# Kernel tuning notes

Measured on AMD Instinct MI355X. Metric: run time of the kernel, lower is better.

## Reference

```python
import jax, jax.numpy as jnp
import numpy as np
from jax import lax

KD, KH, KW = 9, 9, 9  # box-filter window (matches torch ones([1,1,9,9,9]))


def _box_sum(x):
    """Sum over a 9x9x9 window with SAME (zero) padding, via separable 1D convs.
    x: [B, 1, D, H, W]. Mathematically identical to conv3d with an all-ones
    9x9x9 kernel, but O(3k) instead of O(k^3) work per voxel.
    """
    dn = ('NCDHW', 'OIDHW', 'NCDHW')
    dt = x.dtype
    kd = jnp.ones((1, 1, KD, 1, 1), dt)
    kh = jnp.ones((1, 1, 1, KH, 1), dt)
    kw = jnp.ones((1, 1, 1, 1, KW), dt)
    pd, ph, pw = (KD - 1) // 2, (KH - 1) // 2, (KW - 1) // 2
    x = lax.conv_general_dilated(x, kd, (1, 1, 1), [(pd, pd), (0, 0), (0, 0)], dimension_numbers=dn)
    x = lax.conv_general_dilated(x, kh, (1, 1, 1), [(0, 0), (ph, ph), (0, 0)], dimension_numbers=dn)
    x = lax.conv_general_dilated(x, kw, (1, 1, 1), [(0, 0), (0, 0), (pw, pw)], dimension_numbers=dn)
    return x


def setup_inputs() -> dict:
    key = jax.random.key(0)
    k1, k2 = jax.random.split(key)
    shape = (2, 1, 160, 192, 160)  # [B, C=1, D, H, W]
    return {
        'input': jax.random.normal(k1, shape, dtype=jnp.float32),
        'target': jax.random.normal(k2, shape, dtype=jnp.float32),
    }


def reference(input, target):
    ksize = jnp.asarray(KD * KH * KW, input.dtype)
    I_sum = _box_sum(input)
    T_sum = _box_sum(target)
    II_sum = _box_sum(input * input)
    TT_sum = _box_sum(target * target)
    IT_sum = _box_sum(input * target)

    Ihat = I_sum / ksize
    That = T_sum / ksize
    cross = IT_sum - Ihat * T_sum - That * I_sum + That * Ihat * ksize
    T_var = TT_sum - 2 * That * T_sum + That * That * ksize
    I_var = II_sum - 2 * Ihat * I_sum + Ihat * Ihat * ksize
    cc = cross * cross / (T_var * I_var + 1e-5)
    return -1.0 * jnp.mean(cc)
```

## Files before the change

### kernel.cpp

```cpp
#include <hip/hip_runtime.h>

#define DIM_W 160
#define DIM_H 192
#define DIM_D 160
#define DIM_B 2

constexpr int TW = 16;
constexpr int TH = 32;
constexpr int CH = 28;
constexpr int NCH = 6;
constexpr int RH = TH + 8;
constexpr int RWDS = 24;
constexpr float INV_K = 1.0f / 729.0f;
constexpr double NTOT = 9830400.0;

typedef unsigned int u32;
typedef __attribute__((address_space(1))) const u32 gu32;
typedef __attribute__((address_space(3))) u32 lu32;

__global__ void init_kernel(float* out, float* ws) {
    out[0] = 0.0f;
    ws[0] = 0.0f; ws[1] = 0.0f; ws[2] = 0.0f; ws[3] = 0.0f;
}

__device__ __forceinline__ int clampD(int s) {
    return s < 0 ? 0 : (s > DIM_D - 1 ? DIM_D - 1 : s);
}

__global__ __launch_bounds__(256)
void lncc3d_kernel(const float* __restrict__ I,
                   const float* __restrict__ T,
                   const float* __restrict__ zsrc,
                   float* __restrict__ out)
{
    __shared__ __align__(16) float sR[2][2][1024];
    __shared__ __align__(16) float4 wA[RH][16];
    __shared__ __align__(16) float  wB[16][42];
    __shared__ float red[4];

    const int tid  = threadIdx.x;
    const int lane = tid & 63;
    const int wid  = tid >> 6;
    const int wo   = tid & 15;
    const int hb   = (tid >> 4) << 1;

    const int bw = blockIdx.x, bh = blockIdx.y, bz = blockIdx.z;
    const int b  = bz / NCH;
    const int c  = bz - b * NCH;
    const int w0 = bw * TW, h0 = bh * TH, d0 = c * CH;
    const int dEnd = min(d0 + CH, DIM_D);

    const int plane = DIM_H * DIM_W;
    const int fld = wid >> 1;
    const int khi = wid & 1;
    const float* Fb = (fld ? T : I) + (size_t)b * DIM_D * plane;

    int boff[2], ldof[2];
#pragma unroll
    for (int i = 0; i < 2; ++i) {
        const int ck  = (khi << 1) | i;
        const int s16 = ck * 64 + lane;
        const int row = s16 / 6;
        const int q   = s16 - row * 6;
        const int gh  = h0 - 4 + row;
        const int gw  = w0 - 4 + (q << 2);
        ldof[i] = ck << 8;
        boff[i] = (row < RH && gh >= 0 && gh < DIM_H && gw >= 0 && gw <= DIM_W - 4)
                  ? (gh * DIM_W + gw) : -1;
    }

    auto issue = [&](int sc, int buf) {
        const float* Fs = Fb + (size_t)sc * plane;
#pragma unroll
        for (int i = 0; i < 2; ++i) {
            const float* gp = (boff[i] >= 0) ? (Fs + boff[i]) : zsrc;
            __builtin_amdgcn_global_load_lds((gu32*)gp, (lu32*)&sR[buf][fld][ldof[i]],
                                             16, 0, 0);
        }
    };

    float rgI[2][9], rgT[2][9], rgII[2][9], rgTT[2][9], rgIT[2][9];
    float rnI[2], rnT[2], rnII[2], rnTT[2], rnIT[2];
#pragma unroll
    for (int p = 0; p < 2; ++p) {
        rnI[p] = rnT[p] = rnII[p] = rnTT[p] = rnIT[p] = 0.0f;
#pragma unroll
        for (int q = 0; q < 9; ++q) {
            rgI[p][q] = rgT[p][q] = rgII[p][q] = rgTT[p][q] = rgIT[p][q] = 0.0f;
        }
    }
    float acc = 0.0f;

    const int sStart = d0 - 4;
    int cur = 0;

    issue(clampD(sStart), 0);
    issue(clampD(sStart + 1), 1);
    asm volatile("s_waitcnt vmcnt(2)" ::: "memory");
    __builtin_amdgcn_s_barrier();

    for (int t = 0; t < 4; ++t) {
        const int t9 = t * 9;
#pragma unroll
        for (int j = 0; j < 9; ++j) {
            const int s  = sStart + t9 + j;
            const bool vs = (s >= 0) && (s < DIM_D);

            if (vs && tid < 160) {
                const int r  = tid >> 2;
                const int g  = tid & 3;
                const int c0 = g << 2;
                const float* rIp = &sR[cur][0][r * RWDS];
                const float* rTp = &sR[cur][1][r * RWDS];
                const float4 ia  = *(const float4*)(rIp + c0);
                const float4 ib4 = *(const float4*)(rIp + c0 + 4);
                const float4 ic4 = *(const float4*)(rIp + c0 + 8);
                const float4 ta  = *(const float4*)(rTp + c0);
                const float4 tb4 = *(const float4*)(rTp + c0 + 4);
                const float4 tc4 = *(const float4*)(rTp + c0 + 8);
                const float iv[12] = {ia.x, ia.y, ia.z, ia.w, ib4.x, ib4.y, ib4.z, ib4.w,
                                      ic4.x, ic4.y, ic4.z, ic4.w};
                const float tv[12] = {ta.x, ta.y, ta.z, ta.w, tb4.x, tb4.y, tb4.z, tb4.w,
                                      tc4.x, tc4.y, tc4.z, tc4.w};
                float aI = 0.f, aT = 0.f, aII = 0.f, aTT = 0.f, aIT = 0.f;
#pragma unroll
                for (int k = 0; k < 9; ++k) {
                    aI += iv[k]; aT += tv[k];
                    aII = fmaf(iv[k], iv[k], aII);
                    aTT = fmaf(tv[k], tv[k], aTT);
                    aIT = fmaf(iv[k], tv[k], aIT);
                }
                wA[r][(c0 + r) & 15] = make_float4(aI, aT, aII, aTT);
                wB[c0][r] = aIT;
#pragma unroll
                for (int q = 1; q < 4; ++q) {
                    const float ni = iv[8 + q], oi = iv[q - 1];
                    const float nt = tv[8 + q], ot = tv[q - 1];
                    aI += ni - oi; aT += nt - ot;
                    aII = fmaf(ni, ni, fmaf(oi, -oi, aII));
                    aTT = fmaf(nt, nt, fmaf(ot, -ot, aTT));
                    aIT = fmaf(ni, nt, fmaf(oi, -ot, aIT));
                    wA[r][(c0 + q + r) & 15] = make_float4(aI, aT, aII, aTT);
                    wB[c0 + q][r] = aIT;
                }
            }
            asm volatile("s_waitcnt lgkmcnt(0)" ::: "memory");
            __builtin_amdgcn_s_barrier();

            issue(clampD(s + 2), cur);

            float s2I0, s2T0, s2II0, s2TT0, s2IT0, s2I1, s2T1, s2II1, s2TT1, s2IT1;
            if (vs) {
                const float4 A0 = wA[hb][(wo + hb) & 15];
                float sx = A0.x, sy = A0.y, szv = A0.z, swv = A0.w;
#pragma unroll
                for (int k = 1; k < 9; ++k) {
                    const float4 Ak = wA[hb + k][(wo + hb + k) & 15];
                    sx += Ak.x; sy += Ak.y; szv += Ak.z; swv += Ak.w;
                }
                const float4 A9 = wA[hb + 9][(wo + hb + 9) & 15];
                const float2 B0 = *(const float2*)&wB[wo][hb];
                const float2 B1 = *(const float2*)&wB[wo][hb + 2];
                const float2 B2 = *(const float2*)&wB[wo][hb + 4];
                const float2 B3 = *(const float2*)&wB[wo][hb + 6];
                const float2 B4 = *(const float2*)&wB[wo][hb + 8];
                const float sbv = B0.x + B0.y + B1.x + B1.y + B2.x + B2.y
                                + B3.x + B3.y + B4.x;
                s2I0 = sx; s2T0 = sy; s2II0 = szv; s2TT0 = swv; s2IT0 = sbv;
                s2I1  = sx  - A0.x + A9.x;
                s2T1  = sy  - A0.y + A9.y;
                s2II1 = szv - A0.z + A9.z;
                s2TT1 = swv - A0.w + A9.w;
                s2IT1 = sbv - B0.x + B4.y;
            } else {
                s2I0 = s2T0 = s2II0 = s2TT0 = s2IT0 = 0.f;
                s2I1 = s2T1 = s2II1 = s2TT1 = s2IT1 = 0.f;
            }

            rnI[0]  += s2I0  - rgI[0][j];  rgI[0][j]  = s2I0;
            rnT[0]  += s2T0  - rgT[0][j];  rgT[0][j]  = s2T0;
            rnII[0] += s2II0 - rgII[0][j]; rgII[0][j] = s2II0;
            rnTT[0] += s2TT0 - rgTT[0][j]; rgTT[0][j] = s2TT0;
            rnIT[0] += s2IT0 - rgIT[0][j]; rgIT[0][j] = s2IT0;
            rnI[1]  += s2I1  - rgI[1][j];  rgI[1][j]  = s2I1;
            rnT[1]  += s2T1  - rgT[1][j];  rgT[1][j]  = s2T1;
            rnII[1] += s2II1 - rgII[1][j]; rgII[1][j] = s2II1;
            rnTT[1] += s2TT1 - rgTT[1][j]; rgTT[1][j] = s2TT1;
            rnIT[1] += s2IT1 - rgIT[1][j]; rgIT[1][j] = s2IT1;

            if ((s >= d0 + 4) && ((s - 4) < dEnd)) {
                float cr, vv, tvv;
                cr  = rnIT[0] - rnI[0] * rnT[0] * INV_K;
                vv  = rnII[0] - rnI[0] * rnI[0] * INV_K;
                tvv = rnTT[0] - rnT[0] * rnT[0] * INV_K;
                acc += cr * cr * __builtin_amdgcn_rcpf(fmaf(tvv, vv, 1e-5f));
                cr  = rnIT[1] - rnI[1] * rnT[1] * INV_K;
                vv  = rnII[1] - rnI[1] * rnI[1] * INV_K;
                tvv = rnTT[1] - rnT[1] * rnT[1] * INV_K;
                acc += cr * cr * __builtin_amdgcn_rcpf(fmaf(tvv, vv, 1e-5f));
            }

            asm volatile("s_waitcnt lgkmcnt(0)" ::: "memory");
            asm volatile("s_waitcnt vmcnt(2)" ::: "memory");
            __builtin_amdgcn_s_barrier();
            cur ^= 1;
        }
    }

#pragma unroll
    for (int off = 32; off > 0; off >>= 1) acc += __shfl_down(acc, off, 64);
    if (lane == 0) red[wid] = acc;
    __syncthreads();
    if (tid == 0) {
        const float bs = red[0] + red[1] + red[2] + red[3];
        atomicAdd(out, bs * (float)(-1.0 / NTOT));
    }
}

extern "C" void kernel_launch(void* const* d_in, const int* in_sizes, int n_in,
                              void* d_out, int out_size, void* d_ws, size_t ws_size,
                              hipStream_t stream) {
    const float* I = (const float*)d_in[0];
    const float* T = (const float*)d_in[1];
    float* out = (float*)d_out;
    float* ws  = (float*)d_ws;

    init_kernel<<<dim3(1), dim3(1), 0, stream>>>(out, ws);

    dim3 grid(DIM_W / TW, DIM_H / TH, DIM_B * NCH);
    dim3 block(256);
    lncc3d_kernel<<<grid, block, 0, stream>>>(I, T, ws, out);
}
```

Measured before the change: 86.33 us.

## Use DPP prefix-scan for H-direction box sum and retile blocks

Result: slower. 91.99 us (+6.6%).

```diff
diff --git a/kernel.cpp b/kernel.cpp
--- a/kernel.cpp
+++ b/kernel.cpp
@@ -6,10 +6,10 @@
 #define DIM_B 2
 
 constexpr int TW = 16;
-constexpr int TH = 32;
-constexpr int CH = 28;
-constexpr int NCH = 6;
-constexpr int RH = TH + 8;
+constexpr int TH = 24;
+constexpr int CH = 19;
+constexpr int NCH = 9;
+constexpr int RH = 32;
 constexpr int RWDS = 24;
 constexpr float INV_K = 1.0f / 729.0f;
 constexpr double NTOT = 9830400.0;
@@ -26,6 +26,23 @@
 __device__ __forceinline__ int clampD(int s) {
     return s < 0 ? 0 : (s > DIM_D - 1 ? DIM_D - 1 : s);
 }
+
+#define DPPF(v, ctrl) __builtin_bit_cast(float, \
+    __builtin_amdgcn_update_dpp(0, __builtin_bit_cast(int, (float)(v)), \
+                                (ctrl), 0xF, 0xF, true))
+
+#define SCAN5(S1, S2, S4, S8, SL4) \
+    _Pragma("unroll") \
+    for (int f = 0; f < 5; ++f) { \
+        float L = r0v[f] + r1v[f]; \
+        L += DPPF(L, S1); L += DPPF(L, S2); \
+        L += DPPF(L, S4); L += DPPF(L, S8); \
+        const float Pp4 = DPPF(L, SL4); \
+        const float Pm1 = DPPF(L, S1); \
+        const float r9v = DPPF(r1v[f], SL4); \
+        w0v[f] = Pp4 - r9v - Pm1; \
+        w1v[f] = Pp4 - Pm1 - r0v[f]; \
+    }
 
 __global__ __launch_bounds__(256)
 void lncc3d_kernel(const float* __restrict__ I,
@@ -33,16 +50,16 @@
                    const float* __restrict__ zsrc,
                    float* __restrict__ out)
 {
-    __shared__ __align__(16) float sR[2][2][1024];
+    __shared__ __align__(16) float sR[2][2][768];
     __shared__ __align__(16) float4 wA[RH][16];
-    __shared__ __align__(16) float  wB[16][42];
+    __shared__ __align__(16) float  wB[16][34];
     __shared__ float red[4];
 
     const int tid  = threadIdx.x;
     const int lane = tid & 63;
     const int wid  = tid >> 6;
-    const int wo   = tid & 15;
-    const int hb   = (tid >> 4) << 1;
+    const int wo   = tid >> 4;
+    const int i    = tid & 15;
 
     const int bw = blockIdx.x, bh = blockIdx.y, bz = blockIdx.z;
     const int b  = bz / NCH;
@@ -51,42 +68,47 @@
     const int dEnd = min(d0 + CH, DIM_D);
 
     const int plane = DIM_H * DIM_W;
-    const int fld = wid >> 1;
-    const int khi = wid & 1;
-    const float* Fb = (fld ? T : I) + (size_t)b * DIM_D * plane;
-
-    int boff[2], ldof[2];
-#pragma unroll
-    for (int i = 0; i < 2; ++i) {
-        const int ck  = (khi << 1) | i;
-        const int s16 = ck * 64 + lane;
+    const float* Ib = I + (size_t)b * DIM_D * plane;
+    const float* Tb = T + (size_t)b * DIM_D * plane;
+
+    const int shp = __builtin_amdgcn_update_dpp(0, lane, 0x104, 0xF, 0xF, true);
+    const bool dirA = (__builtin_amdgcn_readfirstlane(shp) == 4);
+
+    const bool ldw = (wid >= 2);
+    const int  fldg = (wid == 3);
+    const float* Fbg = fldg ? Tb : Ib;
+    int goff[3];
+#pragma unroll
+    for (int kk = 0; kk < 3; ++kk) {
+        const int s16 = kk * 64 + lane;
         const int row = s16 / 6;
         const int q   = s16 - row * 6;
         const int gh  = h0 - 4 + row;
         const int gw  = w0 - 4 + (q << 2);
-        ldof[i] = ck << 8;
-        boff[i] = (row < RH && gh >= 0 && gh < DIM_H && gw >= 0 && gw <= DIM_W - 4)
-                  ? (gh * DIM_W + gw) : -1;
+        goff[kk] = (gh >= 0 && gh < DIM_H && gw >= 0 && gw <= DIM_W - 4)
+                   ? (gh * DIM_W + gw) : -1;
     }
 
     auto issue = [&](int sc, int buf) {
-        const float* Fs = Fb + (size_t)sc * plane;
-#pragma unroll
-        for (int i = 0; i < 2; ++i) {
-            const float* gp = (boff[i] >= 0) ? (Fs + boff[i]) : zsrc;
-            __builtin_amdgcn_global_load_lds((gu32*)gp, (lu32*)&sR[buf][fld][ldof[i]],
-                                             16, 0, 0);
+        if (ldw) {
+            const float* Fs = Fbg + (size_t)sc * plane;
+#pragma unroll
+            for (int kk = 0; kk < 3; ++kk) {
+                const float* gp = (goff[kk] >= 0) ? (Fs + goff[kk]) : zsrc;
+                __builtin_amdgcn_global_load_lds((gu32*)gp,
+                    (lu32*)&sR[buf][fldg][kk << 8], 16, 0, 0);
+            }
         }
     };
 
-    float rgI[2][9], rgT[2][9], rgII[2][9], rgTT[2][9], rgIT[2][9];
-    float rnI[2], rnT[2], rnII[2], rnTT[2], rnIT[2];
+    float rg[2][5][9], rn[2][5];
 #pragma unroll
     for (int p = 0; p < 2; ++p) {
-        rnI[p] = rnT[p] = rnII[p] = rnTT[p] = rnIT[p] = 0.0f;
-#pragma unroll
-        for (int q = 0; q < 9; ++q) {
-            rgI[p][q] = rgT[p][q] = rgII[p][q] = rgTT[p][q] = rgIT[p][q] = 0.0f;
+#pragma unroll
+        for (int f = 0; f < 5; ++f) {
+            rn[p][f] = 0.0f;
+#pragma unroll
+            for (int q = 0; q < 9; ++q) rg[p][f][q] = 0.0f;
         }
     }
     float acc = 0.0f;
@@ -96,20 +118,21 @@
 
     issue(clampD(sStart), 0);
     issue(clampD(sStart + 1), 1);
-    asm volatile("s_waitcnt vmcnt(2)" ::: "memory");
+    if (ldw) { asm volatile("s_waitcnt vmcnt(3)" ::: "memory"); }
     __builtin_amdgcn_s_barrier();
 
-    for (int t = 0; t < 4; ++t) {
+    for (int t = 0; t < 3; ++t) {
         const int t9 = t * 9;
 #pragma unroll
         for (int j = 0; j < 9; ++j) {
             const int s  = sStart + t9 + j;
             const bool vs = (s >= 0) && (s < DIM_D);
 
-            if (vs && tid < 160) {
+            if (vs && tid < 128) {
                 const int r  = tid >> 2;
                 const int g  = tid & 3;
                 const int c0 = g << 2;
+                const int rr = r + (r >> 1);
                 const float* rIp = &sR[cur][0][r * RWDS];
                 const float* rTp = &sR[cur][1][r * RWDS];
                 const float4 ia  = *(const float4*)(rIp + c0);
@@ -130,7 +153,7 @@
                     aTT = fmaf(tv[k], tv[k], aTT);
                     aIT = fmaf(iv[k], tv[k], aIT);
                 }
-                wA[r][(c0 + r) & 15] = make_float4(aI, aT, aII, aTT);
+                wA[r][(c0 + rr) & 15] = make_float4(aI, aT, aII, aTT);
                 wB[c0][r] = aIT;
 #pragma unroll
                 for (int q = 1; q < 4; ++q) {
@@ -140,7 +163,7 @@
                     aII = fmaf(ni, ni, fmaf(oi, -oi, aII));
                     aTT = fmaf(nt, nt, fmaf(ot, -ot, aTT));
                     aIT = fmaf(ni, nt, fmaf(oi, -ot, aIT));
-                    wA[r][(c0 + q + r) & 15] = make_float4(aI, aT, aII, aTT);
+                    wA[r][(c0 + q + rr) & 15] = make_float4(aI, aT, aII, aTT);
                     wB[c0 + q][r] = aIT;
                 }
             }
@@ -149,59 +172,42 @@
 
             issue(clampD(s + 2), cur);
 
-            float s2I0, s2T0, s2II0, s2TT0, s2IT0, s2I1, s2T1, s2II1, s2TT1, s2IT1;
+            float w0v[5], w1v[5];
             if (vs) {
-                const float4 A0 = wA[hb][(wo + hb) & 15];
-                float sx = A0.x, sy = A0.y, szv = A0.z, swv = A0.w;
-#pragma unroll
-                for (int k = 1; k < 9; ++k) {
-                    const float4 Ak = wA[hb + k][(wo + hb + k) & 15];
-                    sx += Ak.x; sy += Ak.y; szv += Ak.z; swv += Ak.w;
-                }
-                const float4 A9 = wA[hb + 9][(wo + hb + 9) & 15];
-                const float2 B0 = *(const float2*)&wB[wo][hb];
-                const float2 B1 = *(const float2*)&wB[wo][hb + 2];
-                const float2 B2 = *(const float2*)&wB[wo][hb + 4];
-                const float2 B3 = *(const float2*)&wB[wo][hb + 6];
-                const float2 B4 = *(const float2*)&wB[wo][hb + 8];
-                const float sbv = B0.x + B0.y + B1.x + B1.y + B2.x + B2.y
-                                + B3.x + B3.y + B4.x;
-                s2I0 = sx; s2T0 = sy; s2II0 = szv; s2TT0 = swv; s2IT0 = sbv;
-                s2I1  = sx  - A0.x + A9.x;
-                s2T1  = sy  - A0.y + A9.y;
-                s2II1 = szv - A0.z + A9.z;
-                s2TT1 = swv - A0.w + A9.w;
-                s2IT1 = sbv - B0.x + B4.y;
+                float r0v[5], r1v[5];
+                const float4 A0 = wA[2 * i][(wo + 3 * i) & 15];
+                const float4 A1 = wA[2 * i + 1][(wo + 3 * i + 1) & 15];
+                const float2 Bv = *(const float2*)&wB[wo][2 * i];
+                r0v[0] = A0.x; r0v[1] = A0.y; r0v[2] = A0.z; r0v[3] = A0.w; r0v[4] = Bv.x;
+                r1v[0] = A1.x; r1v[1] = A1.y; r1v[2] = A1.z; r1v[3] = A1.w; r1v[4] = Bv.y;
+                if (dirA) {
+                    SCAN5(0x111, 0x112, 0x114, 0x118, 0x104)
+                } else {
+                    SCAN5(0x101, 0x102, 0x104, 0x108, 0x114)
+                }
             } else {
-                s2I0 = s2T0 = s2II0 = s2TT0 = s2IT0 = 0.f;
-                s2I1 = s2T1 = s2II1 = s2TT1 = s2IT1 = 0.f;
-            }
-
-            rnI[0]  += s2I0  - rgI[0][j];  rgI[0][j]  = s2I0;
-            rnT[0]  += s2T0  - rgT[0][j];  rgT[0][j]  = s2T0;
-            rnII[0] += s2II0 - rgII[0][j]; rgII[0][j] = s2II0;
-            rnTT[0] += s2TT0 - rgTT[0][j]; rgTT[0][j] = s2TT0;
-            rnIT[0] += s2IT0 - rgIT[0][j]; rgIT[0][j] = s2IT0;
-            rnI[1]  += s2I1  - rgI[1][j];  rgI[1][j]  = s2I1;
-            rnT[1]  += s2T1  - rgT[1][j];  rgT[1][j]  = s2T1;
-            rnII[1] += s2II1 - rgII[1][j]; rgII[1][j] = s2II1;
-            rnTT[1] += s2TT1 - rgTT[1][j]; rgTT[1][j] = s2TT1;
-            rnIT[1] += s2IT1 - rgIT[1][j]; rgIT[1][j] = s2IT1;
-
-            if ((s >= d0 + 4) && ((s - 4) < dEnd)) {
-                float cr, vv, tvv;
-                cr  = rnIT[0] - rnI[0] * rnT[0] * INV_K;
-                vv  = rnII[0] - rnI[0] * rnI[0] * INV_K;
-                tvv = rnTT[0] - rnT[0] * rnT[0] * INV_K;
-                acc += cr * cr * __builtin_amdgcn_rcpf(fmaf(tvv, vv, 1e-5f));
-                cr  = rnIT[1] - rnI[1] * rnT[1] * INV_K;
-                vv  = rnII[1] - rnI[1] * rnI[1] * INV_K;
-                tvv = rnTT[1] - rnT[1] * rnT[1] * INV_K;
-                acc += cr * cr * __builtin_amdgcn_rcpf(fmaf(tvv, vv, 1e-5f));
+#pragma unroll
+                for (int f = 0; f < 5; ++f) { w0v[f] = 0.f; w1v[f] = 0.f; }
+            }
+
+#pragma unroll
+            for (int f = 0; f < 5; ++f) {
+                rn[0][f] += w0v[f] - rg[0][f][j];  rg[0][f][j] = w0v[f];
+                rn[1][f] += w1v[f] - rg[1][f][j];  rg[1][f][j] = w1v[f];
+            }
+
+            if ((s >= d0 + 4) && ((s - 4) < dEnd) && (i < 12)) {
+#pragma unroll
+                for (int p = 0; p < 2; ++p) {
+                    const float cr  = rn[p][4] - rn[p][0] * rn[p][1] * INV_K;
+                    const float vv  = rn[p][2] - rn[p][0] * rn[p][0] * INV_K;
+                    const float tvv = rn[p][3] - rn[p][1] * rn[p][1] * INV_K;
+                    acc += cr * cr * __builtin_amdgcn_rcpf(fmaf(tvv, vv, 1e-5f));
+                }
             }
 
             asm volatile("s_waitcnt lgkmcnt(0)" ::: "memory");
-            asm volatile("s_waitcnt vmcnt(2)" ::: "memory");
+            if (ldw) { asm volatile("s_waitcnt vmcnt(3)" ::: "memory"); }
             __builtin_amdgcn_s_barrier();
             cur ^= 1;
         }
```

## Process two depth slices per barrier step, pack H-stage partials as fp16

Applied to the files above, without the earlier changes.

Result: no change. 85.93 us (-0.5%).

```diff
diff --git a/kernel.cpp b/kernel.cpp
--- a/kernel.cpp
+++ b/kernel.cpp
@@ -7,9 +7,9 @@
 
 constexpr int TW = 16;
 constexpr int TH = 32;
-constexpr int CH = 28;
-constexpr int NCH = 6;
-constexpr int RH = TH + 8;
+constexpr int CH = 19;
+constexpr int NCH = 9;
+constexpr int RH = 40;
 constexpr int RWDS = 24;
 constexpr float INV_K = 1.0f / 729.0f;
 constexpr double NTOT = 9830400.0;
@@ -17,6 +17,7 @@
 typedef unsigned int u32;
 typedef __attribute__((address_space(1))) const u32 gu32;
 typedef __attribute__((address_space(3))) u32 lu32;
+typedef _Float16 h2 __attribute__((ext_vector_type(2)));
 
 __global__ void init_kernel(float* out, float* ws) {
     out[0] = 0.0f;
@@ -26,6 +27,12 @@
 __device__ __forceinline__ int clampD(int s) {
     return s < 0 ? 0 : (s > DIM_D - 1 ? DIM_D - 1 : s);
 }
+
+__device__ __forceinline__ u32 pkf16(float a, float b) {
+    return __builtin_bit_cast(u32, __builtin_amdgcn_cvt_pkrtz(a, b));
+}
+
+struct S2 { float I0, T0, II0, TT0, IT0, I1, T1, II1, TT1, IT1; };
 
 __global__ __launch_bounds__(256)
 void lncc3d_kernel(const float* __restrict__ I,
@@ -33,9 +40,9 @@
                    const float* __restrict__ zsrc,
                    float* __restrict__ out)
 {
-    __shared__ __align__(16) float sR[2][2][1024];
-    __shared__ __align__(16) float4 wA[RH][16];
-    __shared__ __align__(16) float  wB[16][42];
+    __shared__ __align__(16) float sR[2][2][2][1024];
+    __shared__ __align__(16) uint2 wA[2][RH][16];
+    __shared__ __align__(16) float wB[2][16][44];
     __shared__ float red[4];
 
     const int tid  = threadIdx.x;
@@ -51,32 +58,110 @@
     const int dEnd = min(d0 + CH, DIM_D);
 
     const int plane = DIM_H * DIM_W;
-    const int fld = wid >> 1;
-    const int khi = wid & 1;
-    const float* Fb = (fld ? T : I) + (size_t)b * DIM_D * plane;
-
-    int boff[2], ldof[2];
-#pragma unroll
-    for (int i = 0; i < 2; ++i) {
-        const int ck  = (khi << 1) | i;
-        const int s16 = ck * 64 + lane;
+    const float* Ib = I + (size_t)b * DIM_D * plane;
+    const float* Tb = T + (size_t)b * DIM_D * plane;
+
+    const int  sl0  = (tid >= 160) ? 1 : 0;
+    const int  rem0 = tid - (sl0 ? 160 : 0);
+    const int  r0   = rem0 >> 2, g0 = rem0 & 3;
+    const bool has2 = (tid < 64);
+    const int  r1   = 24 + (tid >> 2), g1 = tid & 3;
+
+    const int stg_sl  = wid >> 1;
+    const int stg_fld = wid & 1;
+    const float* Fbg = (stg_fld ? Tb : Ib);
+    int goff[4];
+#pragma unroll
+    for (int k = 0; k < 4; ++k) {
+        const int s16 = k * 64 + lane;
         const int row = s16 / 6;
         const int q   = s16 - row * 6;
         const int gh  = h0 - 4 + row;
         const int gw  = w0 - 4 + (q << 2);
-        ldof[i] = ck << 8;
-        boff[i] = (row < RH && gh >= 0 && gh < DIM_H && gw >= 0 && gw <= DIM_W - 4)
+        goff[k] = (row < RH && gh >= 0 && gh < DIM_H && gw >= 0 && gw <= DIM_W - 4)
                   ? (gh * DIM_W + gw) : -1;
     }
 
-    auto issue = [&](int sc, int buf) {
-        const float* Fs = Fb + (size_t)sc * plane;
-#pragma unroll
-        for (int i = 0; i < 2; ++i) {
-            const float* gp = (boff[i] >= 0) ? (Fs + boff[i]) : zsrc;
-            __builtin_amdgcn_global_load_lds((gu32*)gp, (lu32*)&sR[buf][fld][ldof[i]],
-                                             16, 0, 0);
-        }
+    auto issue = [&](int spair, int buf) {
+        const int sc = clampD(spair + stg_sl);
+        const float* Fs = Fbg + (size_t)sc * plane;
+#pragma unroll
+        for (int k = 0; k < 4; ++k) {
+            const float* gp = (goff[k] >= 0) ? (Fs + goff[k]) : zsrc;
+            __builtin_amdgcn_global_load_lds((gu32*)gp,
+                (lu32*)&sR[buf][stg_sl][stg_fld][k << 8], 16, 0, 0);
+        }
+    };
+
+    auto st1 = [&](int buf, int sl, int r, int g) {
+        const int c0 = g << 2;
+        const float* rIp = &sR[buf][sl][0][r * RWDS];
+        const float* rTp = &sR[buf][sl][1][r * RWDS];
+        const float4 ia  = *(const float4*)(rIp + c0);
+        const float4 ib4 = *(const float4*)(rIp + c0 + 4);
+        const float4 ic4 = *(const float4*)(rIp + c0 + 8);
+        const float4 ta  = *(const float4*)(rTp + c0);
+        const float4 tb4 = *(const float4*)(rTp + c0 + 4);
+        const float4 tc4 = *(const float4*)(rTp + c0 + 8);
+        const float iv[12] = {ia.x, ia.y, ia.z, ia.w, ib4.x, ib4.y, ib4.z, ib4.w,
+                              ic4.x, ic4.y, ic4.z, ic4.w};
+        const float tv[12] = {ta.x, ta.y, ta.z, ta.w, tb4.x, tb4.y, tb4.z, tb4.w,
+                              tc4.x, tc4.y, tc4.z, tc4.w};
+        float aI = 0.f, aT = 0.f, aII = 0.f, aTT = 0.f, aIT = 0.f;
+#pragma unroll
+        for (int k = 0; k < 9; ++k) {
+            aI += iv[k]; aT += tv[k];
+            aII = fmaf(iv[k], iv[k], aII);
+            aTT = fmaf(tv[k], tv[k], aTT);
+            aIT = fmaf(iv[k], tv[k], aIT);
+        }
+        wA[sl][r][(c0 + r) & 15] = make_uint2(pkf16(aI, aT), pkf16(aII, aTT));
+        wB[sl][c0][r] = aIT;
+#pragma unroll
+        for (int q = 1; q < 4; ++q) {
+            const float ni = iv[8 + q], oi = iv[q - 1];
+            const float nt = tv[8 + q], ot = tv[q - 1];
+            aI += ni - oi; aT += nt - ot;
+            aII = fmaf(ni, ni, fmaf(oi, -oi, aII));
+            aTT = fmaf(nt, nt, fmaf(ot, -ot, aTT));
+            aIT = fmaf(ni, nt, fmaf(oi, -ot, aIT));
+            wA[sl][r][(c0 + q + r) & 15] = make_uint2(pkf16(aI, aT), pkf16(aII, aTT));
+            wB[sl][c0 + q][r] = aIT;
+        }
+    };
+
+    auto st2 = [&](int sl, bool vsx) -> S2 {
+        S2 o;
+        if (vsx) {
+            const uint2 C0 = wA[sl][hb][(wo + hb) & 15];
+            const h2 A0a = __builtin_bit_cast(h2, C0.x);
+            const h2 A0b = __builtin_bit_cast(h2, C0.y);
+            h2 SA = A0a, SB = A0b;
+#pragma unroll
+            for (int k = 1; k < 9; ++k) {
+                const uint2 Ck = wA[sl][hb + k][(wo + hb + k) & 15];
+                SA += __builtin_bit_cast(h2, Ck.x);
+                SB += __builtin_bit_cast(h2, Ck.y);
+            }
+            const uint2 C9 = wA[sl][hb + 9][(wo + hb + 9) & 15];
+            const h2 P1A = SA - A0a + __builtin_bit_cast(h2, C9.x);
+            const h2 P1B = SB - A0b + __builtin_bit_cast(h2, C9.y);
+            o.I0 = (float)SA.x;  o.T0 = (float)SA.y;
+            o.II0 = (float)SB.x; o.TT0 = (float)SB.y;
+            o.I1 = (float)P1A.x; o.T1 = (float)P1A.y;
+            o.II1 = (float)P1B.x; o.TT1 = (float)P1B.y;
+            const float2 B0 = *(const float2*)&wB[sl][wo][hb];
+            const float2 B1 = *(const float2*)&wB[sl][wo][hb + 2];
+            const float2 B2 = *(const float2*)&wB[sl][wo][hb + 4];
+            const float2 B3 = *(const float2*)&wB[sl][wo][hb + 6];
+            const float2 B4 = *(const float2*)&wB[sl][wo][hb + 8];
+            o.IT0 = B0.x + B0.y + B1.x + B1.y + B2.x + B2.y + B3.x + B3.y + B4.x;
+            o.IT1 = o.IT0 - B0.x + B4.y;
+        } else {
+            o.I0 = o.T0 = o.II0 = o.TT0 = o.IT0 = 0.f;
+            o.I1 = o.T1 = o.II1 = o.TT1 = o.IT1 = 0.f;
+        }
+        return o;
     };
 
     float rgI[2][9], rgT[2][9], rgII[2][9], rgTT[2][9], rgIT[2][9];
@@ -90,122 +175,69 @@
         }
     }
     float acc = 0.0f;
-
     const int sStart = d0 - 4;
-    int cur = 0;
-
-    issue(clampD(sStart), 0);
-    issue(clampD(sStart + 1), 1);
-    asm volatile("s_waitcnt vmcnt(2)" ::: "memory");
+
+    issue(sStart, 0);
+    issue(sStart + 2, 1);
+    asm volatile("s_waitcnt vmcnt(4)" ::: "memory");
     __builtin_amdgcn_s_barrier();
 
-    for (int t = 0; t < 4; ++t) {
-        const int t9 = t * 9;
-#pragma unroll
-        for (int j = 0; j < 9; ++j) {
-            const int s  = sStart + t9 + j;
-            const bool vs = (s >= 0) && (s < DIM_D);
-
-            if (vs && tid < 160) {
-                const int r  = tid >> 2;
-                const int g  = tid & 3;
-                const int c0 = g << 2;
-                const float* rIp = &sR[cur][0][r * RWDS];
-                const float* rTp = &sR[cur][1][r * RWDS];
-                const float4 ia  = *(const float4*)(rIp + c0);
-                const float4 ib4 = *(const float4*)(rIp + c0 + 4);
-                const float4 ic4 = *(const float4*)(rIp + c0 + 8);
-                const float4 ta  = *(const float4*)(rTp + c0);
-                const float4 tb4 = *(const float4*)(rTp + c0 + 4);
-                const float4 tc4 = *(const float4*)(rTp + c0 + 8);
-                const float iv[12] = {ia.x, ia.y, ia.z, ia.w, ib4.x, ib4.y, ib4.z, ib4.w,
-                                      ic4.x, ic4.y, ic4.z, ic4.w};
-                const float tv[12] = {ta.x, ta.y, ta.z, ta.w, tb4.x, tb4.y, tb4.z, tb4.w,
-                                      tc4.x, tc4.y, tc4.z, tc4.w};
-                float aI = 0.f, aT = 0.f, aII = 0.f, aTT = 0.f, aIT = 0.f;
-#pragma unroll
-                for (int k = 0; k < 9; ++k) {
-                    aI += iv[k]; aT += tv[k];
-                    aII = fmaf(iv[k], iv[k], aII);
-                    aTT = fmaf(tv[k], tv[k], aTT);
-                    aIT = fmaf(iv[k], tv[k], aIT);
-                }
-                wA[r][(c0 + r) & 15] = make_float4(aI, aT, aII, aTT);
-                wB[c0][r] = aIT;
-#pragma unroll
-                for (int q = 1; q < 4; ++q) {
-                    const float ni = iv[8 + q], oi = iv[q - 1];
-                    const float nt = tv[8 + q], ot = tv[q - 1];
-                    aI += ni - oi; aT += nt - ot;
-                    aII = fmaf(ni, ni, fmaf(oi, -oi, aII));
-                    aTT = fmaf(nt, nt, fmaf(ot, -ot, aTT));
-                    aIT = fmaf(ni, nt, fmaf(oi, -ot, aIT));
-                    wA[r][(c0 + q + r) & 15] = make_float4(aI, aT, aII, aTT);
-                    wB[c0 + q][r] = aIT;
-                }
-            }
-            asm volatile("s_waitcnt lgkmcnt(0)" ::: "memory");
-            __builtin_amdgcn_s_barrier();
-
-            issue(clampD(s + 2), cur);
-
-            float s2I0, s2T0, s2II0, s2TT0, s2IT0, s2I1, s2T1, s2II1, s2TT1, s2IT1;
-            if (vs) {
-                const float4 A0 = wA[hb][(wo + hb) & 15];
-                float sx = A0.x, sy = A0.y, szv = A0.z, swv = A0.w;
-#pragma unroll
-                for (int k = 1; k < 9; ++k) {
-                    const float4 Ak = wA[hb + k][(wo + hb + k) & 15];
-                    sx += Ak.x; sy += Ak.y; szv += Ak.z; swv += Ak.w;
-                }
-                const float4 A9 = wA[hb + 9][(wo + hb + 9) & 15];
-                const float2 B0 = *(const float2*)&wB[wo][hb];
-                const float2 B1 = *(const float2*)&wB[wo][hb + 2];
-                const float2 B2 = *(const float2*)&wB[wo][hb + 4];
-                const float2 B3 = *(const float2*)&wB[wo][hb + 6];
-                const float2 B4 = *(const float2*)&wB[wo][hb + 8];
-                const float sbv = B0.x + B0.y + B1.x + B1.y + B2.x + B2.y
-                                + B3.x + B3.y + B4.x;
-                s2I0 = sx; s2T0 = sy; s2II0 = szv; s2TT0 = swv; s2IT0 = sbv;
-                s2I1  = sx  - A0.x + A9.x;
-                s2T1  = sy  - A0.y + A9.y;
-                s2II1 = szv - A0.z + A9.z;
-                s2TT1 = swv - A0.w + A9.w;
-                s2IT1 = sbv - B0.x + B4.y;
-            } else {
-                s2I0 = s2T0 = s2II0 = s2TT0 = s2IT0 = 0.f;
-                s2I1 = s2T1 = s2II1 = s2TT1 = s2IT1 = 0.f;
-            }
-
-            rnI[0]  += s2I0  - rgI[0][j];  rgI[0][j]  = s2I0;
-            rnT[0]  += s2T0  - rgT[0][j];  rgT[0][j]  = s2T0;
-            rnII[0] += s2II0 - rgII[0][j]; rgII[0][j] = s2II0;
-            rnTT[0] += s2TT0 - rgTT[0][j]; rgTT[0][j] = s2TT0;
-            rnIT[0] += s2IT0 - rgIT[0][j]; rgIT[0][j] = s2IT0;
-            rnI[1]  += s2I1  - rgI[1][j];  rgI[1][j]  = s2I1;
-            rnT[1]  += s2T1  - rgT[1][j];  rgT[1][j]  = s2T1;
-            rnII[1] += s2II1 - rgII[1][j]; rgII[1][j] = s2II1;
-            rnTT[1] += s2TT1 - rgTT[1][j]; rgTT[1][j] = s2TT1;
-            rnIT[1] += s2IT1 - rgIT[1][j]; rgIT[1][j] = s2IT1;
-
-            if ((s >= d0 + 4) && ((s - 4) < dEnd)) {
-                float cr, vv, tvv;
-                cr  = rnIT[0] - rnI[0] * rnT[0] * INV_K;
-                vv  = rnII[0] - rnI[0] * rnI[0] * INV_K;
-                tvv = rnTT[0] - rnT[0] * rnT[0] * INV_K;
-                acc += cr * cr * __builtin_amdgcn_rcpf(fmaf(tvv, vv, 1e-5f));
-                cr  = rnIT[1] - rnI[1] * rnT[1] * INV_K;
-                vv  = rnII[1] - rnI[1] * rnI[1] * INV_K;
-                tvv = rnTT[1] - rnT[1] * rnT[1] * INV_K;
-                acc += cr * cr * __builtin_amdgcn_rcpf(fmaf(tvv, vv, 1e-5f));
-            }
-
-            asm volatile("s_waitcnt lgkmcnt(0)" ::: "memory");
-            asm volatile("s_waitcnt vmcnt(2)" ::: "memory");
-            __builtin_amdgcn_s_barrier();
-            cur ^= 1;
-        }
-    }
+#define RING(S, J, EM) { \
+    rnI[0]  += S.I0  - rgI[0][J];  rgI[0][J]  = S.I0; \
+    rnT[0]  += S.T0  - rgT[0][J];  rgT[0][J]  = S.T0; \
+    rnII[0] += S.II0 - rgII[0][J]; rgII[0][J] = S.II0; \
+    rnTT[0] += S.TT0 - rgTT[0][J]; rgTT[0][J] = S.TT0; \
+    rnIT[0] += S.IT0 - rgIT[0][J]; rgIT[0][J] = S.IT0; \
+    rnI[1]  += S.I1  - rgI[1][J];  rgI[1][J]  = S.I1; \
+    rnT[1]  += S.T1  - rgT[1][J];  rgT[1][J]  = S.T1; \
+    rnII[1] += S.II1 - rgII[1][J]; rgII[1][J] = S.II1; \
+    rnTT[1] += S.TT1 - rgTT[1][J]; rgTT[1][J] = S.TT1; \
+    rnIT[1] += S.IT1 - rgIT[1][J]; rgIT[1][J] = S.IT1; \
+    if (EM) { \
+        float cr, vv, tvv; \
+        cr  = rnIT[0] - rnI[0] * rnT[0] * INV_K; \
+        vv  = rnII[0] - rnI[0] * rnI[0] * INV_K; \
+        tvv = rnTT[0] - rnT[0] * rnT[0] * INV_K; \
+        acc += cr * cr * __builtin_amdgcn_rcpf(fmaf(tvv, vv, 1e-5f)); \
+        cr  = rnIT[1] - rnI[1] * rnT[1] * INV_K; \
+        vv  = rnII[1] - rnI[1] * rnI[1] * INV_K; \
+        tvv = rnTT[1] - rnT[1] * rnT[1] * INV_K; \
+        acc += cr * cr * __builtin_amdgcn_rcpf(fmaf(tvv, vv, 1e-5f)); \
+    } }
+
+#define PAIR(PP, J0, J1, BUF) { \
+    const int sA = sStart + 2 * (PP); \
+    const int sB = sA + 1; \
+    const bool vsA = (sA >= 0) && (sA < DIM_D); \
+    const bool vsB = (sB >= 0) && (sB < DIM_D); \
+    const bool v0 = sl0 ? vsB : vsA; \
+    if (v0) st1((BUF), sl0, r0, g0); \
+    if (has2 && vsB) st1((BUF), 1, r1, g1); \
+    asm volatile("s_waitcnt lgkmcnt(0)" ::: "memory"); \
+    __builtin_amdgcn_s_barrier(); \
+    issue(sA + 4, (BUF)); \
+    { \
+        const S2 sa = st2(0, vsA); \
+        const S2 sb = st2(1, vsB); \
+        const bool emA = (sA >= d0 + 4) && ((sA - 4) < dEnd); \
+        const bool emB = (sB >= d0 + 4) && ((sB - 4) < dEnd); \
+        RING(sa, J0, emA); \
+        RING(sb, J1, emB); \
+    } \
+    asm volatile("s_waitcnt lgkmcnt(0)" ::: "memory"); \
+    asm volatile("s_waitcnt vmcnt(4)" ::: "memory"); \
+    __builtin_amdgcn_s_barrier(); \
+}
+
+    PAIR(0,  0, 1, 0)  PAIR(1,  2, 3, 1)  PAIR(2,  4, 5, 0)  PAIR(3,  6, 7, 1)
+    PAIR(4,  8, 0, 0)  PAIR(5,  1, 2, 1)  PAIR(6,  3, 4, 0)  PAIR(7,  5, 6, 1)
+    PAIR(8,  7, 8, 0)  PAIR(9,  0, 1, 1)  PAIR(10, 2, 3, 0)  PAIR(11, 4, 5, 1)
+    PAIR(12, 6, 7, 0)  PAIR(13, 8, 0, 1)
+
+#undef PAIR
+#undef RING
+
+    asm volatile("s_waitcnt vmcnt(0)" ::: "memory");
 
 #pragma unroll
     for (int off = 32; off > 0; off >>= 1) acc += __shfl_down(acc, off, 64);
```

## Store W-sums in packed fp16, shrink depth chunks, raise occupancy

Applied to the files above, without the earlier changes.

Measured after the change: 188.3 us. 118% more time.

```diff
diff --git a/kernel.cpp b/kernel.cpp
--- a/kernel.cpp
+++ b/kernel.cpp
@@ -7,9 +7,9 @@
 
 constexpr int TW = 16;
 constexpr int TH = 32;
-constexpr int CH = 28;
-constexpr int NCH = 6;
-constexpr int RH = TH + 8;
+constexpr int CH = 19;
+constexpr int NCH = 9;
+constexpr int RH = 40;
 constexpr int RWDS = 24;
 constexpr float INV_K = 1.0f / 729.0f;
 constexpr double NTOT = 9830400.0;
@@ -17,6 +17,7 @@
 typedef unsigned int u32;
 typedef __attribute__((address_space(1))) const u32 gu32;
 typedef __attribute__((address_space(3))) u32 lu32;
+typedef _Float16 h2 __attribute__((ext_vector_type(2)));
 
 __global__ void init_kernel(float* out, float* ws) {
     out[0] = 0.0f;
@@ -27,15 +28,19 @@
     return s < 0 ? 0 : (s > DIM_D - 1 ? DIM_D - 1 : s);
 }
 
-__global__ __launch_bounds__(256)
+__device__ __forceinline__ u32 pkf16(float a, float b) {
+    return __builtin_bit_cast(u32, __builtin_amdgcn_cvt_pkrtz(a, b));
+}
+
+__global__ __launch_bounds__(256, 6)
 void lncc3d_kernel(const float* __restrict__ I,
                    const float* __restrict__ T,
                    const float* __restrict__ zsrc,
                    float* __restrict__ out)
 {
     __shared__ __align__(16) float sR[2][2][1024];
-    __shared__ __align__(16) float4 wA[RH][16];
-    __shared__ __align__(16) float  wB[16][42];
+    __shared__ __align__(16) uint2 wA[RH][16];
+    __shared__ __align__(16) float wB[16][44];
     __shared__ float red[4];
 
     const int tid  = threadIdx.x;
@@ -53,7 +58,8 @@
     const int plane = DIM_H * DIM_W;
     const int fld = wid >> 1;
     const int khi = wid & 1;
-    const float* Fb = (fld ? T : I) + (size_t)b * DIM_D * plane;
+    const float* Fb = ((wid & 2) ? T : I) + (size_t)b * DIM_D * plane;
+    (void)fld;
 
     int boff[2], ldof[2];
 #pragma unroll
@@ -74,19 +80,21 @@
 #pragma unroll
         for (int i = 0; i < 2; ++i) {
             const float* gp = (boff[i] >= 0) ? (Fs + boff[i]) : zsrc;
-            __builtin_amdgcn_global_load_lds((gu32*)gp, (lu32*)&sR[buf][fld][ldof[i]],
-                                             16, 0, 0);
+            __builtin_amdgcn_global_load_lds((gu32*)gp,
+                (lu32*)&sR[buf][(wid & 2) >> 1][ldof[i]], 16, 0, 0);
         }
     };
 
-    float rgI[2][9], rgT[2][9], rgII[2][9], rgTT[2][9], rgIT[2][9];
+    const h2 HZ = __builtin_bit_cast(h2, (u32)0);
+    h2 rgA[2][9], rgB[2][9];
+    float rgC[2][9];
     float rnI[2], rnT[2], rnII[2], rnTT[2], rnIT[2];
 #pragma unroll
     for (int p = 0; p < 2; ++p) {
         rnI[p] = rnT[p] = rnII[p] = rnTT[p] = rnIT[p] = 0.0f;
 #pragma unroll
         for (int q = 0; q < 9; ++q) {
-            rgI[p][q] = rgT[p][q] = rgII[p][q] = rgTT[p][q] = rgIT[p][q] = 0.0f;
+            rgA[p][q] = HZ; rgB[p][q] = HZ; rgC[p][q] = 0.0f;
         }
     }
     float acc = 0.0f;
@@ -99,7 +107,7 @@
     asm volatile("s_waitcnt vmcnt(2)" ::: "memory");
     __builtin_amdgcn_s_barrier();
 
-    for (int t = 0; t < 4; ++t) {
+    for (int t = 0; t < 3; ++t) {
         const int t9 = t * 9;
 #pragma unroll
         for (int j = 0; j < 9; ++j) {
@@ -130,7 +138,7 @@
                     aTT = fmaf(tv[k], tv[k], aTT);
                     aIT = fmaf(iv[k], tv[k], aIT);
                 }
-                wA[r][(c0 + r) & 15] = make_float4(aI, aT, aII, aTT);
+                wA[r][(c0 + r) & 15] = make_uint2(pkf16(aI, aT), pkf16(aII, aTT));
                 wB[c0][r] = aIT;
 #pragma unroll
                 for (int q = 1; q < 4; ++q) {
@@ -140,7 +148,7 @@
                     aII = fmaf(ni, ni, fmaf(oi, -oi, aII));
                     aTT = fmaf(nt, nt, fmaf(ot, -ot, aTT));
                     aIT = fmaf(ni, nt, fmaf(oi, -ot, aIT));
-                    wA[r][(c0 + q + r) & 15] = make_float4(aI, aT, aII, aTT);
+                    wA[r][(c0 + q + r) & 15] = make_uint2(pkf16(aI, aT), pkf16(aII, aTT));
                     wB[c0 + q][r] = aIT;
                 }
             }
@@ -149,44 +157,45 @@
 
             issue(clampD(s + 2), cur);
 
-            float s2I0, s2T0, s2II0, s2TT0, s2IT0, s2I1, s2T1, s2II1, s2TT1, s2IT1;
+            h2 SA, SB, PA, PB;
+            float IT0, IT1;
             if (vs) {
-                const float4 A0 = wA[hb][(wo + hb) & 15];
-                float sx = A0.x, sy = A0.y, szv = A0.z, swv = A0.w;
+                const uint2 C0 = wA[hb][(wo + hb) & 15];
+                const h2 A0a = __builtin_bit_cast(h2, C0.x);
+                const h2 A0b = __builtin_bit_cast(h2, C0.y);
+                SA = A0a; SB = A0b;
 #pragma unroll
                 for (int k = 1; k < 9; ++k) {
-                    const float4 Ak = wA[hb + k][(wo + hb + k) & 15];
-                    sx += Ak.x; sy += Ak.y; szv += Ak.z; swv += Ak.w;
+                    const uint2 Ck = wA[hb + k][(wo + hb + k) & 15];
+                    SA += __builtin_bit_cast(h2, Ck.x);
+                    SB += __builtin_bit_cast(h2, Ck.y);
                 }
-                const float4 A9 = wA[hb + 9][(wo + hb + 9) & 15];
+                const uint2 C9 = wA[hb + 9][(wo + hb + 9) & 15];
+                PA = SA - A0a + __builtin_bit_cast(h2, C9.x);
+                PB = SB - A0b + __builtin_bit_cast(h2, C9.y);
                 const float2 B0 = *(const float2*)&wB[wo][hb];
                 const float2 B1 = *(const float2*)&wB[wo][hb + 2];
                 const float2 B2 = *(const float2*)&wB[wo][hb + 4];
                 const float2 B3 = *(const float2*)&wB[wo][hb + 6];
                 const float2 B4 = *(const float2*)&wB[wo][hb + 8];
-                const float sbv = B0.x + B0.y + B1.x + B1.y + B2.x + B2.y
-                                + B3.x + B3.y + B4.x;
-                s2I0 = sx; s2T0 = sy; s2II0 = szv; s2TT0 = swv; s2IT0 = sbv;
-                s2I1  = sx  - A0.x + A9.x;
-                s2T1  = sy  - A0.y + A9.y;
-                s2II1 = szv - A0.z + A9.z;
-                s2TT1 = swv - A0.w + A9.w;
-                s2IT1 = sbv - B0.x + B4.y;
+                IT0 = B0.x + B0.y + B1.x + B1.y + B2.x + B2.y + B3.x + B3.y + B4.x;
+                IT1 = IT0 - B0.x + B4.y;
             } else {
-                s2I0 = s2T0 = s2II0 = s2TT0 = s2IT0 = 0.f;
-                s2I1 = s2T1 = s2II1 = s2TT1 = s2IT1 = 0.f;
+                SA = HZ; SB = HZ; PA = HZ; PB = HZ; IT0 = 0.f; IT1 = 0.f;
             }
 
-            rnI[0]  += s2I0  - rgI[0][j];  rgI[0][j]  = s2I0;
-            rnT[0]  += s2T0  - rgT[0][j];  rgT[0][j]  = s2T0;
-            rnII[0] += s2II0 - rgII[0][j]; rgII[0][j] = s2II0;
-            rnTT[0] += s2TT0 - rgTT[0][j]; rgTT[0][j] = s2TT0;
-            rnIT[0] += s2IT0 - rgIT[0][j]; rgIT[0][j] = s2IT0;
-            rnI[1]  += s2I1  - rgI[1][j];  rgI[1][j]  = s2I1;
-            rnT[1]  += s2T1  - rgT[1][j];  rgT[1][j]  = s2T1;
-            rnII[1] += s2II1 - rgII[1][j]; rgII[1][j] = s2II1;
-            rnTT[1] += s2TT1 - rgTT[1][j]; rgTT[1][j] = s2TT1;
-            rnIT[1] += s2IT1 - rgIT[1][j]; rgIT[1][j] = s2IT1;
+            rnI[0]  += (float)SA.x - (float)rgA[0][j].x;
+            rnT[0]  += (float)SA.y - (float)rgA[0][j].y;
+            rnII[0] += (float)SB.x - (float)rgB[0][j].x;
+            rnTT[0] += (float)SB.y - (float)rgB[0][j].y;
+            rnIT[0] += IT0 - rgC[0][j];
+            rgA[0][j] = SA; rgB[0][j] = SB; rgC[0][j] = IT0;
+            rnI[1]  += (float)PA.x - (float)rgA[1][j].x;
+            rnT[1]  += (float)PA.y - (float)rgA[1][j].y;
+            rnII[1] += (float)PB.x - (float)rgB[1][j].x;
+            rnTT[1] += (float)PB.y - (float)rgB[1][j].y;
+            rnIT[1] += IT1 - rgC[1][j];
+            rgA[1][j] = PA; rgB[1][j] = PB; rgC[1][j] = IT1;
 
             if ((s >= d0 + 4) && ((s - 4) < dEnd)) {
                 float cr, vv, tvv;
@@ -207,6 +216,8 @@
         }
     }
 
+    asm volatile("s_waitcnt vmcnt(0)" ::: "memory");
+
 #pragma unroll
     for (int off = 32; off > 0; off >>= 1) acc += __shfl_down(acc, off, 64);
     if (lane == 0) red[wid] = acc;
```
